# Kernel optimization log

Measured on AMD Instinct MI355X. Metric: run time of the kernel, lower is better.

Reference implementation:

```python
import jax, jax.numpy as jnp
from jax import lax
import numpy as np

Bn, DM, HH, WW = 2, 192, 64, 64   # batch, d_model, H, W (H==W required by transpose-stack)
DI = 384   # d_inner = ssm_ratio * d_model
DS = 16    # ssm_d_state
ND = 4     # n_directions
CG = 12    # c_group
LN_EPS = 1e-5


def setup_inputs() -> dict:
    key = jax.random.key(0)
    k = jax.random.split(key, 16)
    w = lambda i, shape: jax.random.normal(k[i], shape, jnp.float32) * 0.05
    return {
        "x": jax.random.normal(k[0], (Bn, DM, HH, WW), jnp.float32),
        "in_proj_w": w(1, (DI, DM)),
        "dwconv_w": w(2, (DI, 1, 3, 3)),
        "dwconv_b": w(3, (DI,)),
        "x_down_w": w(4, (DS, DI)),
        "w_up_w": w(5, (CG * DI, DS)),
        "l_up_w": w(6, (ND * DI, DS)),
        "u_up_w": w(7, (ND * DI, DS)),
        "d_up_w": w(8, (ND * DI, DS)),
        "m_w": w(9, (ND,)),
        "grn_gamma": w(10, (DI,)),
        "grn_beta": w(11, (DI,)),
        "norm_w": 1.0 + w(12, (DI,)),
        "norm_b": w(13, (DI,)),
        "out_proj_w": w(14, (DM, DI)),
    }


def _conv1x1(w, x):
    return jnp.einsum('oc,bchw->bohw', w, x)


def _gate_recurrent(X, B, G1, G2, G3):
    # H[:, :, h, w] = B*X + G1*H[h-1,w-1] + G2*H[h,w-1] + G3*H[h+1,w-1]
    # sequential over width; vectorized over batch/channel/height via a column scan.
    def step(hprev, col):  # hprev: [B, C, H]
        xw, bw, g1w, g2w, g3w = col
        z = jnp.zeros_like(hprev[:, :, :1])
        up = jnp.concatenate([z, hprev[:, :, :-1]], axis=2)   # H[h-1, w-1]
        dn = jnp.concatenate([hprev[:, :, 1:], z], axis=2)    # H[h+1, w-1]
        h = bw * xw + g1w * up + g2w * hprev + g3w * dn
        return h, h

    cols = tuple(jnp.moveaxis(t, 3, 0) for t in (X, B, G1, G2, G3))  # [W, B, C, H]
    h0 = jnp.zeros(X.shape[:3], X.dtype)
    _, ys = lax.scan(step, h0, cols)
    return jnp.moveaxis(ys, 0, 3)  # [B, C, H, W]


def _normalize_w(Gl, Gm, Gr):
    gl, gm, gr = jax.nn.sigmoid(Gl), jax.nn.sigmoid(Gm), jax.nn.sigmoid(Gr)
    s = gl + gm + gr
    s = s.at[:, :, 0, :].set(gm[:, :, 0, :] + gr[:, :, 0, :])
    s = s.at[:, :, -1, :].set(gl[:, :, -1, :] + gm[:, :, -1, :])
    s = jnp.maximum(s, 1e-7)
    return gl / s, gm / s, gr / s


def reference(x, in_proj_w, dwconv_w, dwconv_b, x_down_w, w_up_w, l_up_w, u_up_w,
              d_up_w, m_w, grn_gamma, grn_beta, norm_w, norm_b, out_proj_w):
    Bsz = x.shape[0]
    # in_proj (1x1, no bias) + SiLU + depthwise 3x3 conv
    h = jax.nn.silu(_conv1x1(in_proj_w, x))
    h = lax.conv_general_dilated(h, dwconv_w, (1, 1), ((1, 1), (1, 1)),
                                 feature_group_count=DI) + dwconv_b[None, :, None, None]
    # forward_corev1
    xp = _conv1x1(x_down_w, h)            # [B, DS, H, W]
    ws = _conv1x1(w_up_w, xp)             # [B, 12*DI, H, W]
    Ls = _conv1x1(l_up_w, xp)             # [B, 4*DI, H, W]
    Us = _conv1x1(u_up_w, xp)
    Ds = _conv1x1(d_up_w, xp)
    hT = jnp.swapaxes(h, 2, 3)            # requires H==W
    xs = jnp.concatenate([h, hT, h[..., ::-1], hT[..., ::-1]], axis=1)  # [B, 4*DI, H, W]
    G1, G2, G3 = jnp.split(ws, 3, axis=1)
    g1, g2, g3 = _normalize_w(G1, G2, G3)
    out = _gate_recurrent(xs, Ls, g1, g2, g3)
    out = out * Us + xs * Ds
    # merge directions: view [B, 4, DI*H, W], 1x1 conv 4->1
    out = out.reshape(Bsz, ND, DI * HH, WW)
    y = jnp.einsum('d,bdxw->bxw', m_w, out).reshape(Bsz, DI, HH, WW)
    # LayerNorm2d over channel dim
    mu = y.mean(axis=1, keepdims=True)
    var = ((y - mu) ** 2).mean(axis=1, keepdims=True)
    y = (y - mu) * lax.rsqrt(var + LN_EPS) * norm_w[None, :, None, None] + norm_b[None, :, None, None]
    # GRN
    Gx = jnp.sqrt(jnp.sum(y * y, axis=(2, 3), keepdims=True))        # [B, C, 1, 1]
    Nx = Gx / (Gx.mean(axis=1, keepdims=True) + 1e-6)
    y = grn_gamma[None, :, None, None] * (y * Nx) + grn_beta[None, :, None, None] + y
    # out_proj (1x1, no bias)
    return _conv1x1(out_proj_w, y)
```

## Files before the change

### kernel.cpp

```cpp
#include <hip/hip_runtime.h>
#include <math.h>

#define Bn 2
#define DM 192
#define DI 384
#define DS 16
#define HH 64
#define WW 64
#define HW 4096
#define ND 4

__device__ __forceinline__ float fastrcp(float x) { return __builtin_amdgcn_rcpf(x); }
__device__ __forceinline__ float fsig(float x) {
    return fastrcp(1.0f + __expf(-x));
}

__global__ __launch_bounds__(256, 3) void k_inproj(const float* __restrict__ x,
                                                   const float* __restrict__ w,
                                                   float* __restrict__ hpre) {
    int og = blockIdx.y, b = blockIdx.z;
    int p = blockIdx.x * 256 + threadIdx.x;
    const float* wr = w + (size_t)og * 16 * DM;
    const float* xb = x + (size_t)b * DM * HW + p;
    float acc[16];
#pragma unroll
    for (int j = 0; j < 16; ++j) acc[j] = 0.f;
    for (int c = 0; c < DM; c += 4) {
        float x0 = xb[(size_t)(c + 0) * HW];
        float x1 = xb[(size_t)(c + 1) * HW];
        float x2 = xb[(size_t)(c + 2) * HW];
        float x3 = xb[(size_t)(c + 3) * HW];
#pragma unroll
        for (int j = 0; j < 16; ++j) {
            const float* wj = wr + j * DM + c;
            acc[j] = fmaf(wj[0], x0, fmaf(wj[1], x1, fmaf(wj[2], x2, fmaf(wj[3], x3, acc[j]))));
        }
    }
    float* hb = hpre + (size_t)b * DI * HW + (size_t)(og * 16) * HW + p;
#pragma unroll
    for (int j = 0; j < 16; ++j) {
        float v = acc[j];
        hb[(size_t)j * HW] = v * fastrcp(1.0f + __expf(-v));
    }
}

__global__ __launch_bounds__(256) void k_dwconv(const float* __restrict__ hpre,
                                                const float* __restrict__ w,
                                                const float* __restrict__ bias,
                                                float* __restrict__ h) {
    int c = blockIdx.y, b = blockIdx.z;
    int p = blockIdx.x * 256 + threadIdx.x;
    int i = p >> 6, j = p & 63;
    const float* wp = w + c * 9;
    const float* src = hpre + ((size_t)b * DI + c) * HW;
    float acc = bias[c];
#pragma unroll
    for (int di = -1; di <= 1; ++di) {
        int ii = i + di;
        if (ii < 0 || ii >= HH) continue;
#pragma unroll
        for (int dj = -1; dj <= 1; ++dj) {
            int jj = j + dj;
            if (jj < 0 || jj >= WW) continue;
            acc = fmaf(wp[(di + 1) * 3 + (dj + 1)], src[ii * WW + jj], acc);
        }
    }
    h[((size_t)b * DI + c) * HW + p] = acc;
}

__global__ __launch_bounds__(256) void k_xdown(const float* __restrict__ h,
                                               const float* __restrict__ w,
                                               float* __restrict__ xpt) {
    __shared__ float red[4][64][17];
    int tid = threadIdx.x;
    int px = tid & 63, cw = tid >> 6;
    int gp = blockIdx.x * 64 + px;
    int b = gp >> 12, p = gp & 4095;
    const float* hb = h + (size_t)b * DI * HW + p;
    int c0 = cw * 96;
    float a[16];
#pragma unroll
    for (int s = 0; s < 16; ++s) a[s] = 0.f;
    for (int cc = 0; cc < 96; cc += 4) {
        float h0 = hb[(size_t)(c0 + cc + 0) * HW];
        float h1 = hb[(size_t)(c0 + cc + 1) * HW];
        float h2 = hb[(size_t)(c0 + cc + 2) * HW];
        float h3 = hb[(size_t)(c0 + cc + 3) * HW];
#pragma unroll
        for (int s = 0; s < 16; ++s) {
            const float* ws = w + (size_t)s * DI + c0 + cc;
            a[s] = fmaf(ws[0], h0, fmaf(ws[1], h1, fmaf(ws[2], h2, fmaf(ws[3], h3, a[s]))));
        }
    }
#pragma unroll
    for (int s = 0; s < 16; ++s) red[cw][px][s] = a[s];
    __syncthreads();
    int sg = tid >> 6;
    float4 r;
    float* o = &r.x;
#pragma unroll
    for (int j = 0; j < 4; ++j) {
        int s = sg * 4 + j;
        o[j] = red[0][px][s] + red[1][px][s] + red[2][px][s] + red[3][px][s];
    }
    *reinterpret_cast<float4*>(xpt + (size_t)gp * 16 + sg * 4) = r;
}

#define DOT16(W, q0, q1, q2, q3) \
    fmaf(W[15], q3.w, fmaf(W[14], q3.z, fmaf(W[13], q3.y, fmaf(W[12], q3.x, \
    fmaf(W[11], q2.w, fmaf(W[10], q2.z, fmaf(W[9],  q2.y, fmaf(W[8],  q2.x, \
    fmaf(W[7],  q1.w, fmaf(W[6],  q1.z, fmaf(W[5],  q1.y, fmaf(W[4],  q1.x, \
    fmaf(W[3],  q0.w, fmaf(W[2],  q0.z, fmaf(W[1],  q0.y, W[0] * q0.x)))))))))))))))

__global__ __launch_bounds__(256, 3) void k_scan(const float* __restrict__ h,
                                                 const float* __restrict__ xpt,
                                                 const float* __restrict__ wup,
                                                 const float* __restrict__ lup,
                                                 const float* __restrict__ uup,
                                                 const float* __restrict__ dup,
                                                 const float* __restrict__ mw,
                                                 float* __restrict__ y) {
    int c = blockIdx.x, b = blockIdx.y;
    int tid = threadIdx.x;
    int d = tid >> 6, hl = tid & 63;

    __shared__ float htile[64][65];
    __shared__ float acc[64][65];

    const float* hb = h + ((size_t)b * DI + c) * HW;
    for (int i = tid; i < HW; i += 256) {
        htile[i >> 6][i & 63] = hb[i];
        acc[i >> 6][i & 63] = 0.f;
    }

    int row = d * DI + c;
    const float* p1 = wup + (size_t)row * DS;
    const float* p2 = wup + (size_t)(4 * DI + row) * DS;
    const float* p3 = wup + (size_t)(8 * DI + row) * DS;
    const float* pL = lup + (size_t)row * DS;
    const float* pU = uup + (size_t)row * DS;
    const float* pD = dup + (size_t)row * DS;
    float md = mw[d];
    float w1[16], w2[16], w3[16], wL[16], wU[16], wD[16];
#pragma unroll
    for (int s = 0; s < 16; ++s) {
        w1[s] = p1[s]; w2[s] = p2[s]; w3[s] = p3[s];
        wL[s] = pL[s]; wU[s] = md * pU[s]; wD[s] = md * pD[s];
    }
#pragma unroll
    for (int s = 0; s < 16; ++s) {
        asm volatile("" : "+v"(w1[s]), "+v"(w2[s]), "+v"(w3[s]),
                          "+v"(wL[s]), "+v"(wU[s]), "+v"(wD[s]));
    }

    int xstep = (d & 1) ? 65 : 1;
    int xbase = (d & 1) ? hl : hl * 65;
    if (d & 2) { xbase += xstep * 63; xstep = -xstep; }
    const float* xptr = &htile[0][0] + xbase;

    int upA = ((hl - 1) & 63) << 2;
    int dnA = ((hl + 1) & 63) << 2;
    bool isTop = (hl == 0), isBot = (hl == 63);

    float* accp = &acc[hl][0];

    const float4* xq = reinterpret_cast<const float4*>(
        xpt + ((size_t)b * HW + (size_t)hl * 64) * DS);

    float hprev = 0.f;

    float4 A0 = xq[0], A1 = xq[1], A2 = xq[2], A3 = xq[3];
    float4 B0, B1, B2, B3;

    __syncthreads();

    auto docol = [&](const float4& q0, const float4& q1, const float4& q2, const float4& q3) {
        float g1 = DOT16(w1, q0, q1, q2, q3);
        float g2 = DOT16(w2, q0, q1, q2, q3);
        float g3 = DOT16(w3, q0, q1, q2, q3);
        float L  = DOT16(wL, q0, q1, q2, q3);
        float U  = DOT16(wU, q0, q1, q2, q3);
        float Dv = DOT16(wD, q0, q1, q2, q3);
        g1 = fsig(g1); g2 = fsig(g2); g3 = fsig(g3);
        float ssum = g2 + (isTop ? 0.f : g1) + (isBot ? 0.f : g3);
        float inv = fastrcp(fmaxf(ssum, 1e-7f));
        float X = *xptr; xptr += xstep;
        float up = __int_as_float(__builtin_amdgcn_ds_bpermute(upA, __float_as_int(hprev)));
        float dn = __int_as_float(__builtin_amdgcn_ds_bpermute(dnA, __float_as_int(hprev)));
        up = isTop ? 0.f : up;
        dn = isBot ? 0.f : dn;
        float hnew = fmaf(L, X, inv * fmaf(g1, up, fmaf(g2, hprev, g3 * dn)));
        hprev = hnew;
        atomicAdd(accp, fmaf(hnew, U, X * Dv));
        accp += 1;
    };

    for (int w = 0; w < 64; w += 2) {
        const float4* pn = xq + (w + 1) * 4;
        B0 = pn[0]; B1 = pn[1]; B2 = pn[2]; B3 = pn[3];
        docol(A0, A1, A2, A3);
        int w2i = (w + 2 < 64) ? w + 2 : 63;
        const float4* pm = xq + w2i * 4;
        A0 = pm[0]; A1 = pm[1]; A2 = pm[2]; A3 = pm[3];
        docol(B0, B1, B2, B3);
    }

    __syncthreads();
    float* yb = y + ((size_t)b * DI + c) * HW;
    for (int i = tid; i < HW; i += 256) yb[i] = acc[i >> 6][i & 63];
}

__global__ __launch_bounds__(256) void k_ln(float* __restrict__ y,
                                            const float* __restrict__ nw,
                                            const float* __restrict__ nb) {
    int lpx = threadIdx.x & 15, chunk = threadIdx.x >> 4;
    int gp = blockIdx.x * 16 + lpx;
    int b = gp >> 12, p = gp & 4095;
    float* yb = y + (size_t)b * DI * HW + p;

    float vv[24];
    float s = 0.f, s2 = 0.f;
#pragma unroll
    for (int ci = 0; ci < 24; ++ci) {
        float v = yb[(size_t)(chunk * 24 + ci) * HW];
        vv[ci] = v;
        s += v;
        s2 = fmaf(v, v, s2);
    }
    __shared__ float S[16][17], S2[16][17];
    S[chunk][lpx] = s;
    S2[chunk][lpx] = s2;
    __syncthreads();
    float ts = 0.f, ts2 = 0.f;
#pragma unroll
    for (int k = 0; k < 16; ++k) { ts += S[k][lpx]; ts2 += S2[k][lpx]; }
    float mu = ts * (1.0f / DI);
    float var = ts2 * (1.0f / DI) - mu * mu;
    float inv = rsqrtf(var + 1e-5f);
#pragma unroll
    for (int ci = 0; ci < 24; ++ci) {
        int cch = chunk * 24 + ci;
        float v = (vv[ci] - mu) * inv;
        yb[(size_t)cch * HW] = fmaf(v, nw[cch], nb[cch]);
    }
}

__global__ __launch_bounds__(256) void k_grnsum(const float* __restrict__ y,
                                                float* __restrict__ gx) {
    int c = blockIdx.x, b = blockIdx.y;
    const float* yb = y + ((size_t)b * DI + c) * HW;
    float s = 0.f;
#pragma unroll 4
    for (int i = threadIdx.x; i < HW; i += 256) {
        float v = yb[i];
        s = fmaf(v, v, s);
    }
#pragma unroll
    for (int o = 32; o > 0; o >>= 1) s += __shfl_down(s, o);
    __shared__ float red[4];
    int wid = threadIdx.x >> 6;
    if ((threadIdx.x & 63) == 0) red[wid] = s;
    __syncthreads();
    if (threadIdx.x == 0) gx[b * DI + c] = sqrtf(red[0] + red[1] + red[2] + red[3]);
}

__global__ __launch_bounds__(256) void k_grnscale(const float* __restrict__ gxv,
                                                  const float* __restrict__ gamma,
                                                  float* __restrict__ sc) {
    int b = blockIdx.x;
    const float* g = gxv + b * DI;
    int cidx = threadIdx.x;
    float gx0 = g[cidx];
    float gx1 = (cidx < DI - 256) ? g[cidx + 256] : 0.f;
    float s = gx0 + gx1;
#pragma unroll
    for (int o = 32; o > 0; o >>= 1) s += __shfl_down(s, o);
    __shared__ float red[4];
    __shared__ float meanv;
    int wid = threadIdx.x >> 6;
    if ((threadIdx.x & 63) == 0) red[wid] = s;
    __syncthreads();
    if (threadIdx.x == 0) meanv = (red[0] + red[1] + red[2] + red[3]) * (1.0f / DI);
    __syncthreads();
    float m = meanv + 1e-6f;
    sc[b * DI + cidx] = 1.0f + gamma[cidx] * (gx0 / m);
    if (cidx < DI - 256)
        sc[b * DI + cidx + 256] = 1.0f + gamma[cidx + 256] * (gx1 / m);
}

__global__ __launch_bounds__(256, 3) void k_outproj(const float* __restrict__ y,
                                                    const float* __restrict__ w,
                                                    const float* __restrict__ sc_all,
                                                    const float* __restrict__ beta,
                                                    float* __restrict__ out) {
    int og = blockIdx.y, b = blockIdx.z;
    int p = blockIdx.x * 256 + threadIdx.x;
    const float* wr = w + (size_t)og * 8 * DI;
    const float* scb = sc_all + b * DI;
    const float* yb = y + (size_t)b * DI * HW + p;
    float acc[8];
#pragma unroll
    for (int j = 0; j < 8; ++j) acc[j] = 0.f;
    for (int c = 0; c < DI; c += 4) {
        float v0 = fmaf(yb[(size_t)(c + 0) * HW], scb[c + 0], beta[c + 0]);
        float v1 = fmaf(yb[(size_t)(c + 1) * HW], scb[c + 1], beta[c + 1]);
        float v2 = fmaf(yb[(size_t)(c + 2) * HW], scb[c + 2], beta[c + 2]);
        float v3 = fmaf(yb[(size_t)(c + 3) * HW], scb[c + 3], beta[c + 3]);
#pragma unroll
        for (int j = 0; j < 8; ++j) {
            const float* wj = wr + j * DI + c;
            acc[j] = fmaf(wj[0], v0, fmaf(wj[1], v1, fmaf(wj[2], v2, fmaf(wj[3], v3, acc[j]))));
        }
    }
    float* ob = out + (size_t)b * DM * HW + (size_t)(og * 8) * HW + p;
#pragma unroll
    for (int j = 0; j < 8; ++j) ob[(size_t)j * HW] = acc[j];
}

extern "C" void kernel_launch(void* const* d_in, const int* in_sizes, int n_in,
                              void* d_out, int out_size, void* d_ws, size_t ws_size,
                              hipStream_t stream) {
    (void)in_sizes; (void)n_in; (void)out_size; (void)ws_size;
    const float* x          = (const float*)d_in[0];
    const float* in_proj_w  = (const float*)d_in[1];
    const float* dwconv_w   = (const float*)d_in[2];
    const float* dwconv_b   = (const float*)d_in[3];
    const float* x_down_w   = (const float*)d_in[4];
    const float* w_up_w     = (const float*)d_in[5];
    const float* l_up_w     = (const float*)d_in[6];
    const float* u_up_w     = (const float*)d_in[7];
    const float* d_up_w     = (const float*)d_in[8];
    const float* m_w        = (const float*)d_in[9];
    const float* grn_gamma  = (const float*)d_in[10];
    const float* grn_beta   = (const float*)d_in[11];
    const float* norm_w     = (const float*)d_in[12];
    const float* norm_b     = (const float*)d_in[13];
    const float* out_proj_w = (const float*)d_in[14];

    float* ws = (float*)d_ws;
    const size_t NBIG = (size_t)Bn * DI * HW;
    float* hpre = ws;
    float* hbuf = ws + NBIG;
    float* xpt  = ws + 2 * NBIG;
    float* gx   = ws + 2 * NBIG + (size_t)Bn * HW * DS;
    float* sc   = gx + Bn * DI;
    float* y    = hpre;

    k_inproj<<<dim3(16, 24, 2), 256, 0, stream>>>(x, in_proj_w, hpre);
    k_dwconv<<<dim3(16, DI, Bn), 256, 0, stream>>>(hpre, dwconv_w, dwconv_b, hbuf);
    k_xdown<<<dim3(128), 256, 0, stream>>>(hbuf, x_down_w, xpt);
    k_scan<<<dim3(DI, Bn), 256, 0, stream>>>(hbuf, xpt, w_up_w, l_up_w, u_up_w,
                                             d_up_w, m_w, y);
    k_ln<<<dim3(512), 256, 0, stream>>>(y, norm_w, norm_b);
    k_grnsum<<<dim3(DI, Bn), 256, 0, stream>>>(y, gx);
    k_grnscale<<<dim3(Bn), 256, 0, stream>>>(gx, grn_gamma, sc);
    k_outproj<<<dim3(16, 24, 2), 256, 0, stream>>>(y, out_proj_w, sc, grn_beta,
                                                   (float*)d_out);
}
```

Before: 224.6 us.

## Transpose xpt layout for coalesced loads and software-pipeline scan recurrence

The projection kernel now writes xpt in a [b][w][quad][h] float4 layout, so in the scan each lane's per-column load of the 16 projected values is coalesced across the 64 height lanes. The scan loop is restructured so the gate dot products and sigmoids for the next column are computed while the ds_bpermute results for the previous hidden state are still in flight. This takes the neighbour-exchange latency off the serial critical path. It also drops the asm volatile register pins on the weights, which gives the compiler freedom but may change register allocation or occupancy.

```diff
diff --git a/kernel.cpp b/kernel.cpp
--- a/kernel.cpp
+++ b/kernel.cpp
@@ -103,7 +103,8 @@
         int s = sg * 4 + j;
         o[j] = red[0][px][s] + red[1][px][s] + red[2][px][s] + red[3][px][s];
     }
-    *reinterpret_cast<float4*>(xpt + (size_t)gp * 16 + sg * 4) = r;
+    int hp = p >> 6, wp_ = p & 63;
+    reinterpret_cast<float4*>(xpt)[(size_t)b * (HW * 4) + (wp_ * 4 + sg) * 64 + hp] = r;
 }
 
 #define DOT16(W, q0, q1, q2, q3) \
@@ -147,11 +148,6 @@
         w1[s] = p1[s]; w2[s] = p2[s]; w3[s] = p3[s];
         wL[s] = pL[s]; wU[s] = md * pU[s]; wD[s] = md * pD[s];
     }
-#pragma unroll
-    for (int s = 0; s < 16; ++s) {
-        asm volatile("" : "+v"(w1[s]), "+v"(w2[s]), "+v"(w3[s]),
-                          "+v"(wL[s]), "+v"(wU[s]), "+v"(wD[s]));
-    }
 
     int xstep = (d & 1) ? 65 : 1;
     int xbase = (d & 1) ? hl : hl * 65;
@@ -164,46 +160,69 @@
 
     float* accp = &acc[hl][0];
 
-    const float4* xq = reinterpret_cast<const float4*>(
-        xpt + ((size_t)b * HW + (size_t)hl * 64) * DS);
-
-    float hprev = 0.f;
-
-    float4 A0 = xq[0], A1 = xq[1], A2 = xq[2], A3 = xq[3];
-    float4 B0, B1, B2, B3;
-
-    __syncthreads();
-
-    auto docol = [&](const float4& q0, const float4& q1, const float4& q2, const float4& q3) {
-        float g1 = DOT16(w1, q0, q1, q2, q3);
-        float g2 = DOT16(w2, q0, q1, q2, q3);
-        float g3 = DOT16(w3, q0, q1, q2, q3);
-        float L  = DOT16(wL, q0, q1, q2, q3);
-        float U  = DOT16(wU, q0, q1, q2, q3);
-        float Dv = DOT16(wD, q0, q1, q2, q3);
-        g1 = fsig(g1); g2 = fsig(g2); g3 = fsig(g3);
-        float ssum = g2 + (isTop ? 0.f : g1) + (isBot ? 0.f : g3);
-        float inv = fastrcp(fmaxf(ssum, 1e-7f));
-        float X = *xptr; xptr += xstep;
-        float up = __int_as_float(__builtin_amdgcn_ds_bpermute(upA, __float_as_int(hprev)));
-        float dn = __int_as_float(__builtin_amdgcn_ds_bpermute(dnA, __float_as_int(hprev)));
-        up = isTop ? 0.f : up;
-        dn = isBot ? 0.f : dn;
-        float hnew = fmaf(L, X, inv * fmaf(g1, up, fmaf(g2, hprev, g3 * dn)));
-        hprev = hnew;
-        atomicAdd(accp, fmaf(hnew, U, X * Dv));
-        accp += 1;
-    };
-
-    for (int w = 0; w < 64; w += 2) {
-        const float4* pn = xq + (w + 1) * 4;
-        B0 = pn[0]; B1 = pn[1]; B2 = pn[2]; B3 = pn[3];
-        docol(A0, A1, A2, A3);
-        int w2i = (w + 2 < 64) ? w + 2 : 63;
-        const float4* pm = xq + w2i * 4;
-        A0 = pm[0]; A1 = pm[1]; A2 = pm[2]; A3 = pm[3];
-        docol(B0, B1, B2, B3);
-    }
+    const float4* xg = reinterpret_cast<const float4*>(xpt) + (size_t)b * (HW * 4) + hl;
+
+#define LOADQ(R0, R1, R2, R3, wcol) { \
+    const float4* pp_ = xg + (size_t)(wcol) * 256; \
+    R0 = pp_[0]; R1 = pp_[64]; R2 = pp_[128]; R3 = pp_[192]; }
+
+#define PREP(g1S, g2S, g3S, invS, LS, US, DvS, XS, Q0, Q1, Q2, Q3) { \
+    g1S = DOT16(w1, Q0, Q1, Q2, Q3); \
+    g2S = DOT16(w2, Q0, Q1, Q2, Q3); \
+    g3S = DOT16(w3, Q0, Q1, Q2, Q3); \
+    LS  = DOT16(wL, Q0, Q1, Q2, Q3); \
+    US  = DOT16(wU, Q0, Q1, Q2, Q3); \
+    DvS = DOT16(wD, Q0, Q1, Q2, Q3); \
+    g1S = fsig(g1S); g2S = fsig(g2S); g3S = fsig(g3S); \
+    float ss_ = g2S + (isTop ? 0.f : g1S) + (isBot ? 0.f : g3S); \
+    invS = fastrcp(fmaxf(ss_, 1e-7f)); \
+    XS = *xptr; xptr += xstep; }
+
+#define COMB(g1S, g2S, g3S, invS, LS, US, DvS, XS) { \
+    float upv_ = isTop ? 0.f : __int_as_float(upr); \
+    float dnv_ = isBot ? 0.f : __int_as_float(dnr); \
+    float hnew_ = fmaf(LS, XS, invS * fmaf(g1S, upv_, fmaf(g2S, hprev, g3S * dnv_))); \
+    atomicAdd(accp, fmaf(hnew_, US, XS * DvS)); accp += 1; \
+    hprev = hnew_; \
+    upr = __builtin_amdgcn_ds_bpermute(upA, __float_as_int(hprev)); \
+    dnr = __builtin_amdgcn_ds_bpermute(dnA, __float_as_int(hprev)); }
+
+    float4 A0, A1, A2, A3, B0, B1, B2, B3;
+    float g1a, g2a, g3a, inva, La, Ua, Dva, Xa;
+    float g1b, g2b, g3b, invb, Lb, Ub, Dvb, Xb;
+    int upr, dnr;
+    float hprev;
+
+    LOADQ(A0, A1, A2, A3, 0);
+    __syncthreads();
+
+    PREP(g1a, g2a, g3a, inva, La, Ua, Dva, Xa, A0, A1, A2, A3);
+    LOADQ(A0, A1, A2, A3, 1);
+    hprev = La * Xa;
+    atomicAdd(accp, fmaf(hprev, Ua, Xa * Dva)); accp += 1;
+    upr = __builtin_amdgcn_ds_bpermute(upA, __float_as_int(hprev));
+    dnr = __builtin_amdgcn_ds_bpermute(dnA, __float_as_int(hprev));
+    LOADQ(B0, B1, B2, B3, 2);
+
+    for (int w = 1; w < 63; w += 2) {
+        PREP(g1b, g2b, g3b, invb, Lb, Ub, Dvb, Xb, A0, A1, A2, A3);
+        LOADQ(A0, A1, A2, A3, w + 2);
+        COMB(g1b, g2b, g3b, invb, Lb, Ub, Dvb, Xb);
+        PREP(g1a, g2a, g3a, inva, La, Ua, Dva, Xa, B0, B1, B2, B3);
+        int wn = (w + 3 < 64) ? w + 3 : 63;
+        LOADQ(B0, B1, B2, B3, wn);
+        COMB(g1a, g2a, g3a, inva, La, Ua, Dva, Xa);
+    }
+    PREP(g1b, g2b, g3b, invb, Lb, Ub, Dvb, Xb, A0, A1, A2, A3);
+    {
+        float upv_ = isTop ? 0.f : __int_as_float(upr);
+        float dnv_ = isBot ? 0.f : __int_as_float(dnr);
+        float hnew_ = fmaf(Lb, Xb, invb * fmaf(g1b, upv_, fmaf(g2b, hprev, g3b * dnv_)));
+        atomicAdd(accp, fmaf(hnew_, Ub, Xb * Dvb));
+    }
+#undef LOADQ
+#undef PREP
+#undef COMB
 
     __syncthreads();
     float* yb = y + ((size_t)b * DI + c) * HW;
```

Result: faster. 207.1 us (-7.8%).
